# Kernel optimization log

Hardware: AMD Instinct MI355X
Metric: run time of the kernel (lower is better)

Reference implementation:

```python
import jax, jax.numpy as jnp
import numpy as np

ALPHA, BETA, BASE, MARGIN = 2.0, 50.0, 0.5, 0.1
B, D, N_CLASSES = 8192, 128, 512


def setup_inputs() -> dict:
    key = jax.random.key(0)
    k1, k2 = jax.random.split(key)
    emb = jax.random.normal(k1, (B, D), dtype=jnp.float32)
    emb = emb / jnp.linalg.norm(emb, axis=1, keepdims=True)  # L2-normalized as documented
    labels = jax.random.randint(k2, (B,), 0, N_CLASSES, dtype=jnp.int32)
    return {"embeddings": emb, "labels": labels}


def reference(embeddings, labels):
    sim = embeddings @ embeddings.T  # (B, B)
    b = embeddings.shape[0]
    same = labels[:, None] == labels[None, :]
    eye = jnp.eye(b, dtype=bool)
    pos_mask = same & ~eye
    neg_mask = ~same

    # per-row extrema over masked entries (inf sentinels make empty rows inert)
    pos_min = jnp.min(jnp.where(pos_mask, sim, jnp.inf), axis=1)   # (B,)
    neg_max = jnp.max(jnp.where(neg_mask, sim, -jnp.inf), axis=1)  # (B,)

    # hard-pair mining
    hard_pos = pos_mask & (sim - MARGIN < neg_max[:, None])
    hard_neg = neg_mask & (sim + MARGIN > pos_min[:, None])

    valid = (pos_mask.any(axis=1) & neg_mask.any(axis=1)
             & hard_pos.any(axis=1) & hard_neg.any(axis=1))

    pos_sum = jnp.sum(jnp.where(hard_pos, jnp.exp(-ALPHA * (sim - BASE)), 0.0), axis=1)
    neg_sum = jnp.sum(jnp.where(hard_neg, jnp.exp(BETA * (sim - BASE)), 0.0), axis=1)
    row_loss = jnp.log1p(pos_sum) / ALPHA + jnp.log1p(neg_sum) / BETA

    n_valid = jnp.sum(valid)
    loss = jnp.sum(jnp.where(valid, row_loss, 0.0)) / jnp.maximum(n_valid, 1).astype(row_loss.dtype)
    return loss
```

## Files before the change

### kernel.cpp

```cpp
#include <hip/hip_runtime.h>
#include <hip/hip_bf16.h>

#define NB 8192
#define ND 128
#define STR 4

static constexpr float F_ALPHA  = 2.0f;
static constexpr float F_BETA   = 50.0f;
static constexpr float F_BASE   = 0.5f;
static constexpr float F_MARGIN = 0.1f;
static constexpr float LOG2E    = 1.4426950408889634f;
static constexpr float C1P = -F_ALPHA * LOG2E, C0P =  F_ALPHA * F_BASE * LOG2E;
static constexpr float C1N =  F_BETA  * LOG2E, C0N = -F_BETA  * F_BASE * LOG2E;

typedef __attribute__((ext_vector_type(8))) short short8;
typedef __attribute__((ext_vector_type(4))) float f32x4;

__device__ __forceinline__ unsigned fenc(float f) {
  unsigned u = __float_as_uint(f);
  return (u & 0x80000000u) ? ~u : (u | 0x80000000u);
}
__device__ __forceinline__ float fdec(unsigned k) {
  unsigned u = (k & 0x80000000u) ? (k & 0x7FFFFFFFu) : ~k;
  return __uint_as_float(u);
}

__device__ __forceinline__ void async16(const void* g, void* l) {
  __builtin_amdgcn_global_load_lds(
      (const __attribute__((address_space(1))) void*)g,
      (__attribute__((address_space(3))) void*)l, 16, 0, 0);
}

__global__ void k_convert(const float4* __restrict__ in, char* __restrict__ P,
                          const int* __restrict__ lab,
                          unsigned* __restrict__ pmKey, unsigned* __restrict__ nmKey,
                          float* __restrict__ pSum, float* __restrict__ nSum,
                          int* __restrict__ cnt) {
  int i = blockIdx.x * 256 + threadIdx.x;
  float4 v = in[i];
  __hip_bfloat16 a = __float2bfloat16(v.x), b = __float2bfloat16(v.y),
                 c = __float2bfloat16(v.z), d = __float2bfloat16(v.w);
  ushort4 o;
  o.x = *(unsigned short*)&a; o.y = *(unsigned short*)&b;
  o.z = *(unsigned short*)&c; o.w = *(unsigned short*)&d;
  const int row = i >> 5, c4 = i & 31;
  const int g = row >> 4, r15 = row & 15;
  const int kk = c4 >> 3, q = (c4 >> 1) & 3, j = (c4 & 1) * 4;
  *(ushort4*)(P + (((g * 4 + kk) * 64 + q * 16 + r15) * 16 + j * 2)) = o;
  if (i < NB) {
    pmKey[i * STR] = 0xFFFFFFFFu;
    nmKey[i * STR] = 0u;
    pSum[i * STR]  = 0.f;
    nSum[i * STR]  = 0.f;
    atomicAdd(&cnt[lab[i]], 1);
  }
}

template<int PASS>
__global__ __launch_bounds__(256, 2)
void k_simpass(const char* __restrict__ P,
               const int* __restrict__ lab,
               unsigned* __restrict__ pmKey,
               unsigned* __restrict__ nmKey,
               float* __restrict__ pSum,
               float* __restrict__ nSum,
               float* __restrict__ selfSim)
{
  __shared__ __align__(16) char sB[2][8192];

  const int t    = threadIdx.x;
  const int lane = t & 63, wid = t >> 6;
  const int q    = lane >> 4, r15 = lane & 15;
  const int rBase = blockIdx.y * 128 + wid * 32;
  const int cBase = blockIdx.x * 256;

  const char* gB = P + (size_t)cBase * 256;

  async16(gB + wid * 1024 + lane * 16,        &sB[0][0] + wid * 1024);
  async16(gB + 4096 + wid * 1024 + lane * 16, &sB[0][0] + 4096 + wid * 1024);

  short8 afr[4][2];
#pragma unroll
  for (int mi = 0; mi < 2; ++mi) {
    const char* pa = P + (size_t)(((rBase >> 4) + mi) * 4) * 1024 + lane * 16;
#pragma unroll
    for (int kk = 0; kk < 4; ++kk)
      afr[kk][mi] = *(const short8*)(pa + kk * 1024);
  }

  int lrr[8]; float pmr[8], nmr[8];
#pragma unroll
  for (int mi = 0; mi < 2; ++mi)
#pragma unroll
    for (int rg = 0; rg < 4; ++rg) {
      int r = rBase + mi * 16 + q * 4 + rg;
      lrr[mi * 4 + rg] = lab[r];
      if (PASS == 1) {
        pmr[mi * 4 + rg] = fdec(pmKey[r * STR]) - F_MARGIN;
        nmr[mi * 4 + rg] = fdec(nmKey[r * STR]) + F_MARGIN;
      }
    }

  float st1[8], st2[8];
#pragma unroll
  for (int i = 0; i < 8; ++i) {
    st1[i] = (PASS == 0) ?  __builtin_inff() : 0.f;
    st2[i] = (PASS == 0) ? -__builtin_inff() : 0.f;
  }

  int clN0 = lab[cBase + r15];
  int clN1 = lab[cBase + 16 + r15];

  const f32x4 Z4 = (f32x4){0.f, 0.f, 0.f, 0.f};

  __syncthreads();

#pragma unroll 1
  for (int ct = 0; ct < 8; ++ct) {
    const int buf = ct & 1;
    const int cTile = cBase + ct * 32;

    if (ct < 7) {
      const char* gn = gB + (size_t)(ct + 1) * 8192;
      async16(gn + wid * 1024 + lane * 16,        &sB[buf ^ 1][0] + wid * 1024);
      async16(gn + 4096 + wid * 1024 + lane * 16, &sB[buf ^ 1][0] + 4096 + wid * 1024);
    }

    const char* sb = &sB[buf][0] + lane * 16;
    short8 b[8];
#pragma unroll
    for (int kk = 0; kk < 4; ++kk) {
      b[kk]     = *(const short8*)(sb + kk * 1024);
      b[4 + kk] = *(const short8*)(sb + 4096 + kk * 1024);
    }

    f32x4 acc[2][2];
#pragma unroll
    for (int mi = 0; mi < 2; ++mi) {
      acc[mi][0] = __builtin_amdgcn_mfma_f32_16x16x32_bf16(afr[0][mi], b[0], Z4, 0, 0, 0);
      acc[mi][1] = __builtin_amdgcn_mfma_f32_16x16x32_bf16(afr[0][mi], b[4], Z4, 0, 0, 0);
    }
#pragma unroll
    for (int kk = 1; kk < 4; ++kk)
#pragma unroll
      for (int mi = 0; mi < 2; ++mi) {
        acc[mi][0] = __builtin_amdgcn_mfma_f32_16x16x32_bf16(afr[kk][mi], b[kk],     acc[mi][0], 0, 0, 0);
        acc[mi][1] = __builtin_amdgcn_mfma_f32_16x16x32_bf16(afr[kk][mi], b[4 + kk], acc[mi][1], 0, 0, 0);
      }

    const int cl0 = clN0, cl1 = clN1;
    if (ct < 7) {
      clN0 = lab[cTile + 32 + r15];
      clN1 = lab[cTile + 48 + r15];
    }

#pragma unroll
    for (int mi = 0; mi < 2; ++mi)
#pragma unroll
      for (int rg = 0; rg < 4; ++rg) {
        const int idx = mi * 4 + rg;
        const int lr  = lrr[idx];
        const float s0 = acc[mi][0][rg], s1 = acc[mi][1][rg];
        const bool same0 = (lr == cl0), same1 = (lr == cl1);
        if (PASS == 0) {
          float x0 = same0 ? s0 :  __builtin_inff();
          float x1 = same1 ? s1 :  __builtin_inff();
          st1[idx] = fminf(fminf(st1[idx], x0), x1);
          float y0 = same0 ? -__builtin_inff() : s0;
          float y1 = same1 ? -__builtin_inff() : s1;
          st2[idx] = fmaxf(fmaxf(st2[idx], y0), y1);
        } else {
          float e0 = __builtin_amdgcn_exp2f(
              fmaf(s0, same0 ? C1P : C1N, same0 ? C0P : C0N));
          float e1 = __builtin_amdgcn_exp2f(
              fmaf(s1, same1 ? C1P : C1N, same1 ? C0P : C0N));
          bool hp0 = same0 && (s0 < nmr[idx]), hn0 = !same0 && (s0 > pmr[idx]);
          bool hp1 = same1 && (s1 < nmr[idx]), hn1 = !same1 && (s1 > pmr[idx]);
          st1[idx] += (hp0 ? e0 : 0.f) + (hp1 ? e1 : 0.f);
          st2[idx] += (hn0 ? e0 : 0.f) + (hn1 ? e1 : 0.f);
        }
      }

    if (PASS == 0 && cTile == rBase) {
#pragma unroll
      for (int mi = 0; mi < 2; ++mi)
#pragma unroll
        for (int rg = 0; rg < 4; ++rg)
          if (r15 == q * 4 + rg)
            selfSim[rBase + mi * 16 + q * 4 + rg] = acc[mi][mi][rg];
    }

    __syncthreads();
  }

#pragma unroll
  for (int mi = 0; mi < 2; ++mi)
#pragma unroll
    for (int rg = 0; rg < 4; ++rg) {
      const int idx = mi * 4 + rg;
      const int r   = rBase + mi * 16 + q * 4 + rg;
      float v1 = st1[idx], v2 = st2[idx];
      if (PASS == 0) {
#pragma unroll
        for (int d = 1; d < 16; d <<= 1) {
          v1 = fminf(v1, __shfl_xor(v1, d));
          v2 = fmaxf(v2, __shfl_xor(v2, d));
        }
        if (r15 == 0) {
          atomicMin(&pmKey[r * STR], fenc(v1));
          atomicMax(&nmKey[r * STR], fenc(v2));
        }
      } else {
#pragma unroll
        for (int d = 1; d < 16; d <<= 1) {
          v1 += __shfl_xor(v1, d);
          v2 += __shfl_xor(v2, d);
        }
        if (r15 == 0) {
          if (v1 != 0.f) atomicAdd(&pSum[r * STR], v1);
          if (v2 != 0.f) atomicAdd(&nSum[r * STR], v2);
        }
      }
    }
}

__global__ void k_final(const unsigned* __restrict__ pmKey,
                        const unsigned* __restrict__ nmKey,
                        const float* __restrict__ pSum,
                        const float* __restrict__ nSum,
                        const float* __restrict__ selfSim,
                        const int* __restrict__ lab,
                        const int* __restrict__ cnt,
                        float* __restrict__ out)
{
  const int t = threadIdx.x;
  float ls = 0.f, nv = 0.f;
  for (int r = t; r < NB; r += 1024) {
    int c = cnt[lab[r]];
    unsigned nk = nmKey[r * STR];
    bool pe = (c > 1);
    bool ne = (c < NB) && (nk > 0x007FFFFFu);
    if (pe && ne) {
      float pm = fdec(pmKey[r * STR]), nm = fdec(nk);
      if (pm - F_MARGIN < nm) {
        float ss = selfSim[r];
        float psub = (ss - F_MARGIN < nm)
                       ? __builtin_amdgcn_exp2f(fmaf(ss, C1P, C0P)) : 0.f;
        float ps = fmaxf(pSum[r * STR] - psub, 0.f);
        ls += log1pf(ps) * (1.0f / F_ALPHA) + log1pf(nSum[r * STR]) * (1.0f / F_BETA);
        nv += 1.f;
      }
    }
  }
#pragma unroll
  for (int d = 1; d < 64; d <<= 1) {
    ls += __shfl_xor(ls, d);
    nv += __shfl_xor(nv, d);
  }
  __shared__ float sL[16], sC[16];
  if ((t & 63) == 0) { sL[t >> 6] = ls; sC[t >> 6] = nv; }
  __syncthreads();
  if (t == 0) {
    float a = 0.f, c = 0.f;
#pragma unroll
    for (int w = 0; w < 16; ++w) { a += sL[w]; c += sC[w]; }
    out[0] = a / fmaxf(c, 1.f);
  }
}

extern "C" void kernel_launch(void* const* d_in, const int* in_sizes, int n_in,
                              void* d_out, int out_size, void* d_ws, size_t ws_size,
                              hipStream_t stream)
{
  const float* emb = (const float*)d_in[0];
  const int*   lab = (const int*)d_in[1];
  float* out = (float*)d_out;

  char* ws = (char*)d_ws;
  char*     P       = ws;
  unsigned* pmKey   = (unsigned*)(ws + 2097152);
  unsigned* nmKey   = (unsigned*)(ws + 2097152 + 131072);
  float*    pSum    = (float*)(ws + 2097152 + 262144);
  float*    nSum    = (float*)(ws + 2097152 + 393216);
  float*    selfSim = (float*)(ws + 2097152 + 524288);
  int*      cnt     = (int*)(ws + 2097152 + 557056);

  hipMemsetAsync(cnt, 0, 512 * sizeof(int), stream);
  k_convert<<<NB * ND / (256 * 4), 256, 0, stream>>>(
      (const float4*)emb, P, lab, pmKey, nmKey, pSum, nSum, cnt);

  dim3 grid(32, 64);
  k_simpass<0><<<grid, 256, 0, stream>>>(P, lab, pmKey, nmKey, pSum, nSum, selfSim);
  k_simpass<1><<<grid, 256, 0, stream>>>(P, lab, pmKey, nmKey, pSum, nSum, selfSim);
  k_final<<<1, 1024, 0, stream>>>(pmKey, nmKey, pSum, nSum, selfSim, lab, cnt, out);
}
```

Measured before the change: 113.6 us.

## Software-pipeline MFMA with epilogue fold and double per-block column span

```diff
diff --git a/kernel.cpp b/kernel.cpp
--- a/kernel.cpp
+++ b/kernel.cpp
@@ -72,12 +72,14 @@
   const int lane = t & 63, wid = t >> 6;
   const int q    = lane >> 4, r15 = lane & 15;
   const int rBase = blockIdx.y * 128 + wid * 32;
-  const int cBase = blockIdx.x * 256;
+  const int cBase = blockIdx.x * 512;
 
   const char* gB = P + (size_t)cBase * 256;
 
   async16(gB + wid * 1024 + lane * 16,        &sB[0][0] + wid * 1024);
   async16(gB + 4096 + wid * 1024 + lane * 16, &sB[0][0] + 4096 + wid * 1024);
+  async16(gB + 8192 + wid * 1024 + lane * 16, &sB[1][0] + wid * 1024);
+  async16(gB + 12288 + wid * 1024 + lane * 16, &sB[1][0] + 4096 + wid * 1024);
 
   short8 afr[4][2];
 #pragma unroll
@@ -108,33 +110,16 @@
     st2[i] = (PASS == 0) ? -__builtin_inff() : 0.f;
   }
 
-  int clN0 = lab[cBase + r15];
-  int clN1 = lab[cBase + 16 + r15];
-
   const f32x4 Z4 = (f32x4){0.f, 0.f, 0.f, 0.f};
 
-  __syncthreads();
-
-#pragma unroll 1
-  for (int ct = 0; ct < 8; ++ct) {
-    const int buf = ct & 1;
-    const int cTile = cBase + ct * 32;
-
-    if (ct < 7) {
-      const char* gn = gB + (size_t)(ct + 1) * 8192;
-      async16(gn + wid * 1024 + lane * 16,        &sB[buf ^ 1][0] + wid * 1024);
-      async16(gn + 4096 + wid * 1024 + lane * 16, &sB[buf ^ 1][0] + 4096 + wid * 1024);
-    }
-
-    const char* sb = &sB[buf][0] + lane * 16;
+  auto mma = [&](f32x4 (&acc)[2][2], const char* bufBase) {
+    const char* sb = bufBase + lane * 16;
     short8 b[8];
 #pragma unroll
     for (int kk = 0; kk < 4; ++kk) {
       b[kk]     = *(const short8*)(sb + kk * 1024);
       b[4 + kk] = *(const short8*)(sb + 4096 + kk * 1024);
     }
-
-    f32x4 acc[2][2];
 #pragma unroll
     for (int mi = 0; mi < 2; ++mi) {
       acc[mi][0] = __builtin_amdgcn_mfma_f32_16x16x32_bf16(afr[0][mi], b[0], Z4, 0, 0, 0);
@@ -147,13 +132,9 @@
         acc[mi][0] = __builtin_amdgcn_mfma_f32_16x16x32_bf16(afr[kk][mi], b[kk],     acc[mi][0], 0, 0, 0);
         acc[mi][1] = __builtin_amdgcn_mfma_f32_16x16x32_bf16(afr[kk][mi], b[4 + kk], acc[mi][1], 0, 0, 0);
       }
-
-    const int cl0 = clN0, cl1 = clN1;
-    if (ct < 7) {
-      clN0 = lab[cTile + 32 + r15];
-      clN1 = lab[cTile + 48 + r15];
-    }
-
+  };
+
+  auto fold = [&](const f32x4 (&acc)[2][2], int cl0, int cl1, int tl) {
 #pragma unroll
     for (int mi = 0; mi < 2; ++mi)
 #pragma unroll
@@ -180,8 +161,7 @@
           st2[idx] += (hn0 ? e0 : 0.f) + (hn1 ? e1 : 0.f);
         }
       }
-
-    if (PASS == 0 && cTile == rBase) {
+    if (PASS == 0 && cBase + tl * 32 == rBase) {
 #pragma unroll
       for (int mi = 0; mi < 2; ++mi)
 #pragma unroll
@@ -189,9 +169,52 @@
           if (r15 == q * 4 + rg)
             selfSim[rBase + mi * 16 + q * 4 + rg] = acc[mi][mi][rg];
     }
-
-    __syncthreads();
-  }
+  };
+
+  auto stage = [&](int idx, char* buf) {
+    const char* gn = gB + (size_t)idx * 8192;
+    async16(gn + wid * 1024 + lane * 16,        buf + wid * 1024);
+    async16(gn + 4096 + wid * 1024 + lane * 16, buf + 4096 + wid * 1024);
+  };
+
+  f32x4 accA[2][2], accB[2][2];
+  int clP0 = lab[cBase + r15];
+  int clP1 = lab[cBase + 16 + r15];
+  int clC0 = lab[cBase + 32 + r15];
+  int clC1 = lab[cBase + 48 + r15];
+
+  __syncthreads();
+
+  stage(2, &sB[0][0]);
+  mma(accA, &sB[0][0]);
+  __syncthreads();
+
+#pragma unroll 1
+  for (int p = 0; p < 7; ++p) {
+    {
+      const int tc = 2 * p + 1;
+      mma(accB, &sB[1][0]);
+      if (tc + 1 <= 15) stage(tc + 1, &sB[0][0]);
+      fold(accA, clP0, clP1, tc - 1);
+      clP0 = clC0; clP1 = clC1;
+      clC0 = lab[cBase + (tc + 1) * 32 + r15];
+      clC1 = lab[cBase + (tc + 1) * 32 + 16 + r15];
+      __syncthreads();
+    }
+    {
+      const int tc = 2 * p + 2;
+      mma(accA, &sB[0][0]);
+      if (tc + 1 <= 15) stage(tc + 1, &sB[1][0]);
+      fold(accB, clP0, clP1, tc - 1);
+      clP0 = clC0; clP1 = clC1;
+      clC0 = lab[cBase + (tc + 1) * 32 + r15];
+      clC1 = lab[cBase + (tc + 1) * 32 + 16 + r15];
+      __syncthreads();
+    }
+  }
+  mma(accB, &sB[1][0]);
+  fold(accA, clP0, clP1, 14);
+  fold(accB, clC0, clC1, 15);
 
 #pragma unroll
   for (int mi = 0; mi < 2; ++mi)
@@ -289,7 +312,7 @@
   k_convert<<<NB * ND / (256 * 4), 256, 0, stream>>>(
       (const float4*)emb, P, lab, pmKey, nmKey, pSum, nSum, cnt);
 
-  dim3 grid(32, 64);
+  dim3 grid(16, 64);
   k_simpass<0><<<grid, 256, 0, stream>>>(P, lab, pmKey, nmKey, pSum, nSum, selfSim);
   k_simpass<1><<<grid, 256, 0, stream>>>(P, lab, pmKey, nmKey, pSum, nSum, selfSim);
   k_final<<<1, 1024, 0, stream>>>(pmKey, nmKey, pSum, nSum, selfSim, lab, cnt, out);
```

Result: faster. 100.2 us (-11.8%).
